# Optimization experiments

Measured on AMD Instinct MI355X. Metric: run time of the kernel, lower is better.

The kernel has to match this reference:

```python
import jax, jax.numpy as jnp
import numpy as np

F_IN = 22 * 1000   # flattened EEG trial
D_DENSE = 100      # Dense(100) -> becomes T=100 timesteps of dim 1
H = 128            # LSTM units
N_CLASS = 4


def setup_inputs() -> dict:
    key = jax.random.key(0)
    ks = jax.random.split(key, 8)
    B = 4096
    s1 = 1.0 / np.sqrt(F_IN)
    sr = 1.0 / np.sqrt(H)
    x = jax.random.normal(ks[0], (B, 22, 1000), dtype=jnp.float32)
    W1 = jax.random.uniform(ks[1], (F_IN, D_DENSE), jnp.float32, -s1, s1)
    b1 = jnp.zeros((D_DENSE,), jnp.float32)
    # Keras LSTM kernels: input kernel [1, 4H], recurrent kernel [H, 4H], bias [4H]
    Wk = jax.random.uniform(ks[2], (1, 4 * H), jnp.float32, -1.0, 1.0)
    Wr = jax.random.normal(ks[3], (H, 4 * H), dtype=jnp.float32) * sr
    # Keras unit_forget_bias: f-gate bias initialized to 1
    bl = jnp.concatenate([jnp.zeros(H), jnp.ones(H), jnp.zeros(2 * H)]).astype(jnp.float32)
    W2 = jax.random.uniform(ks[4], (H, N_CLASS), jnp.float32, -sr, sr)
    b2 = jnp.zeros((N_CLASS,), jnp.float32)
    return {"x": x, "W1": W1, "b1": b1, "Wk": Wk, "Wr": Wr, "bl": bl, "W2": W2, "b2": b2}


def _lstm_last(seq, Wk, Wr, bl):
    # seq: [B, T, 1]; returns final hidden state [B, H]
    B = seq.shape[0]
    # precompute input contribution for all steps: [T, B, 4H]
    zx = jnp.einsum('btf,fg->tbg', seq, Wk) + bl

    def step(carry, zxt):
        h, c = carry
        z = zxt + h @ Wr                      # [B, 4H]
        i, f, g, o = jnp.split(z, 4, axis=-1)  # keras gate order: i, f, c, o
        i = jax.nn.sigmoid(i)
        f = jax.nn.sigmoid(f)
        g = jnp.tanh(g)
        o = jax.nn.sigmoid(o)
        c = f * c + i * g
        h = o * jnp.tanh(c)
        return (h, c), None

    init = (jnp.zeros((B, H), seq.dtype), jnp.zeros((B, H), seq.dtype))
    (h, _), _ = jax.lax.scan(step, init, zx)
    return h


def reference(x, W1, b1, Wk, Wr, bl, W2, b2):
    B = x.shape[0]
    flat = x.reshape(B, -1)                 # Flatten
    d = flat @ W1 + b1                      # Dense(100), linear activation
    seq = d.reshape(B, D_DENSE, 1)          # Reshape((100, 1))
    h = _lstm_last(seq, Wk, Wr, bl)         # LSTM(128) -> last hidden state
    logits = h @ W2 + b2                    # Dense(4)
    return jax.nn.softmax(logits, axis=-1)
```

## Files before the change

### kernel.cpp

```cpp
#include <hip/hip_runtime.h>
#include <stdint.h>

#define F_IN   22000
#define B_SZ   4096
#define T_STEPS 100
#define NSPLIT 16
#define NCHUNK 22
#define KSPAN  (NCHUNK * 64)
#define ACC_STRIDE 104
#define PART_BYTES ((size_t)NSPLIT * B_SZ * ACC_STRIDE * 4)
#define BIMG_BYTES 28672
#define BIMG_HALF  14336
#define W1IMG_BYTES ((size_t)NSPLIT * NCHUNK * BIMG_BYTES)
#define WRIMG_BYTES (128 * 1024)
#define LOG2E  1.44269504f
#define LOG2E2 2.88539008f

typedef float f32x4 __attribute__((ext_vector_type(4)));
typedef short s16x8 __attribute__((ext_vector_type(8)));

__device__ inline unsigned short f2bf(float f){
  unsigned u = __builtin_bit_cast(unsigned, f);
  u += 0x7FFFu + ((u >> 16) & 1u);
  return (unsigned short)(u >> 16);
}
__device__ inline float bf2f(unsigned short h){
  return __builtin_bit_cast(float, ((unsigned)h) << 16);
}
__device__ inline float exp2f_(float x){
  float r; asm("v_exp_f32 %0, %1" : "=v"(r) : "v"(x)); return r;
}

__global__ __launch_bounds__(256) void k_prep(const float* __restrict__ W1,
                                              const float* __restrict__ Wr,
                                              char* __restrict__ img,
                                              char* __restrict__ wrimg){
  __shared__ float tile[64][129];
  int b = blockIdx.x, tid = threadIdx.x;
  if (b < 352){
    int ch = b % NCHUNK, s = b / NCHUNK;
    int k0 = s * KSPAN + ch * 64;
    char* base = img + ((size_t)(s * NCHUNK + ch)) * BIMG_BYTES;
    for (int idx = tid; idx < 64 * 128; idx += 256){
      int k = idx >> 7, c = idx & 127;
      float v = 0.f;
      if (c < 100 && (k0 + k) < F_IN) v = W1[(size_t)(k0 + k) * 100 + c];
      tile[k][c] = v;
    }
    __syncthreads();
    #pragma unroll
    for (int q = 0; q < 4; ++q){
      int task = q * 256 + tid;
      if (task < 896){
        int p  = task * 16;
        int c  = p >> 7;
        int k8 = ((p >> 4) & 7) ^ (c & 7);
        unsigned hw[4], lw[4];
        #pragma unroll
        for (int jj = 0; jj < 4; ++jj){
          float v0 = tile[k8 * 8 + jj * 2][c];
          float v1 = tile[k8 * 8 + jj * 2 + 1][c];
          unsigned short h0 = f2bf(v0), l0 = f2bf(v0 - bf2f(h0));
          unsigned short h1 = f2bf(v1), l1 = f2bf(v1 - bf2f(h1));
          hw[jj] = (unsigned)h0 | ((unsigned)h1 << 16);
          lw[jj] = (unsigned)l0 | ((unsigned)l1 << 16);
        }
        *(uint4*)(base + p)             = make_uint4(hw[0], hw[1], hw[2], hw[3]);
        *(uint4*)(base + BIMG_HALF + p) = make_uint4(lw[0], lw[1], lw[2], lw[3]);
      }
    }
  } else {
    int gid = (b - 352) * 256 + tid;
    int lane = gid & 63, slot = gid >> 6;
    int kk = slot & 3, G = (slot >> 2) & 3, w = slot >> 4;
    int oct = lane >> 4, lr = lane & 15;
    int col = G * 128 + w * 16 + lr;
    float sg = (G == 2) ? LOG2E2 : LOG2E;
    unsigned pk[4];
    #pragma unroll
    for (int jj = 0; jj < 4; ++jj){
      float v0 = Wr[(size_t)(kk * 32 + oct * 8 + jj * 2)     * 512 + col] * sg;
      float v1 = Wr[(size_t)(kk * 32 + oct * 8 + jj * 2 + 1) * 512 + col] * sg;
      pk[jj] = (unsigned)f2bf(v0) | ((unsigned)f2bf(v1) << 16);
    }
    *(uint4*)(wrimg + (size_t)gid * 16) = make_uint4(pk[0], pk[1], pk[2], pk[3]);
  }
}

__global__ __launch_bounds__(256, 4) void k_dense(const float* __restrict__ x,
                                                  const char* __restrict__ img,
                                                  float* __restrict__ part){
  __shared__ char Bb[BIMG_BYTES];
  int tid = threadIdx.x;
  int lane = tid & 63, w = tid >> 6;
  int r = lane & 15, oct = lane >> 4;
  int brow = blockIdx.x * 64;
  int s = blockIdx.y;
  int arow = brow + w * 16 + r;
  const float* xrow = x + (size_t)arow * F_IN;
  const char* isrc = img + (size_t)s * NCHUNK * BIMG_BYTES;
  int kbase = s * KSPAN;

  f32x4 acc[7];
  #pragma unroll
  for (int i = 0; i < 7; ++i) acc[i] = (f32x4)0.f;

  for (int ch = 0; ch < NCHUNK; ++ch){
    int k0 = kbase + ch * 64;
    int ka0 = k0 + oct * 8;
    int ka1 = k0 + 32 + oct * 8;
    float4 a0 = make_float4(0.f,0.f,0.f,0.f), a1 = a0, a2 = a0, a3 = a0;
    if (ka0 < F_IN){ a0 = *(const float4*)(xrow + ka0);
                     a1 = *(const float4*)(xrow + ka0 + 4); }
    if (ka1 < F_IN){ a2 = *(const float4*)(xrow + ka1);
                     a3 = *(const float4*)(xrow + ka1 + 4); }
    {
      const char* src = isrc + (size_t)ch * BIMG_BYTES;
      #pragma unroll
      for (int i = 0; i < 7; ++i){
        int seg = i * 4 + w;
        __builtin_amdgcn_global_load_lds(
          (const __attribute__((address_space(1))) void*)(src + seg * 1024 + lane * 16),
          (__attribute__((address_space(3))) void*)(Bb + seg * 1024), 16, 0, 0);
      }
    }
    __syncthreads();
    float va[16] = {a0.x,a0.y,a0.z,a0.w, a1.x,a1.y,a1.z,a1.w,
                    a2.x,a2.y,a2.z,a2.w, a3.x,a3.y,a3.z,a3.w};
    s16x8 ah0, al0, ah1, al1;
    #pragma unroll
    for (int j = 0; j < 8; ++j){
      unsigned short h = f2bf(va[j]);
      ah0[j] = (short)h; al0[j] = (short)f2bf(va[j] - bf2f(h));
    }
    #pragma unroll
    for (int j = 0; j < 8; ++j){
      unsigned short h = f2bf(va[8 + j]);
      ah1[j] = (short)h; al1[j] = (short)f2bf(va[8 + j] - bf2f(h));
    }
    #pragma unroll
    for (int ct = 0; ct < 7; ++ct){
      int c = ct * 16 + r;
      int byte0 = ((c * 128 + oct * 16) ^ ((c & 7) << 4));
      int byte1 = ((c * 128 + 64 + oct * 16) ^ ((c & 7) << 4));
      s16x8 bh0 = *(s16x8*)(Bb + byte0);
      s16x8 bl0 = *(s16x8*)(Bb + BIMG_HALF + byte0);
      s16x8 bh1 = *(s16x8*)(Bb + byte1);
      s16x8 bl1 = *(s16x8*)(Bb + BIMG_HALF + byte1);
      acc[ct] = __builtin_amdgcn_mfma_f32_16x16x32_bf16(ah0, bh0, acc[ct], 0, 0, 0);
      acc[ct] = __builtin_amdgcn_mfma_f32_16x16x32_bf16(ah0, bl0, acc[ct], 0, 0, 0);
      acc[ct] = __builtin_amdgcn_mfma_f32_16x16x32_bf16(al0, bh0, acc[ct], 0, 0, 0);
      acc[ct] = __builtin_amdgcn_mfma_f32_16x16x32_bf16(ah1, bh1, acc[ct], 0, 0, 0);
      acc[ct] = __builtin_amdgcn_mfma_f32_16x16x32_bf16(ah1, bl1, acc[ct], 0, 0, 0);
      acc[ct] = __builtin_amdgcn_mfma_f32_16x16x32_bf16(al1, bh1, acc[ct], 0, 0, 0);
    }
    __syncthreads();
  }

  float* pbase = part + (size_t)s * B_SZ * ACC_STRIDE;
  #pragma unroll
  for (int ct = 0; ct < 7; ++ct){
    int col = ct * 16 + r;
    if (col < 100){
      #pragma unroll
      for (int reg = 0; reg < 4; ++reg){
        int orow = brow + w * 16 + oct * 4 + reg;
        pbase[(size_t)orow * ACC_STRIDE + col] = acc[ct][reg];
      }
    }
  }
}

__global__ __launch_bounds__(512, 2) void k_lstm(const float* __restrict__ part,
                                                 const float* __restrict__ b1,
                                                 const float* __restrict__ Wk,
                                                 const char* __restrict__ wrimg,
                                                 const float* __restrict__ bl,
                                                 const float* __restrict__ W2,
                                                 const float* __restrict__ b2,
                                                 float* __restrict__ out){
  __shared__ unsigned short hbuf[2][16 * 128];
  __shared__ float dld[16][ACC_STRIDE];
  __shared__ float hf[16][132];
  int tid = threadIdx.x;
  int lane = tid & 63, w = tid >> 6;
  int oct = lane >> 4, lr = lane & 15;
  int brow = blockIdx.x * 16;

  for (int i = tid; i < 2048; i += 512) hbuf[0][i] = 0;
  for (int i = tid; i < 16 * T_STEPS; i += 512){
    int r = i / T_STEPS, t = i % T_STEPS;
    float v = b1[t];
    #pragma unroll
    for (int s = 0; s < NSPLIT; ++s)
      v += part[((size_t)(s * B_SZ + brow + r)) * ACC_STRIDE + t];
    dld[r][t] = v;
  }

  float wkv[4], blv[4];
  s16x8 bfrag[4][4];
  #pragma unroll
  for (int G = 0; G < 4; ++G){
    int col = G * 128 + w * 16 + lr;
    float sg = (G == 2) ? LOG2E2 : LOG2E;
    wkv[G] = Wk[col] * sg;
    blv[G] = bl[col] * sg;
    #pragma unroll
    for (int kk = 0; kk < 4; ++kk){
      bfrag[G][kk] = *(const s16x8*)(wrimg +
          ((size_t)(((w * 4 + G) * 4 + kk) * 64 + lane)) * 16);
    }
  }
  float cst[4];
  #pragma unroll
  for (int reg = 0; reg < 4; ++reg) cst[reg] = 0.f;
  int sxl = (2 * (((lr >> 2) + (lr & 3)) & 3) + ((lr >> 2) & 1)) << 4;
  __syncthreads();

  for (int t = 0; t < T_STEPS; ++t){
    int cur = t & 1;
    f32x4 accA[4], accB[4];
    float dv[4];
    #pragma unroll
    for (int reg = 0; reg < 4; ++reg) dv[reg] = dld[oct * 4 + reg][t];
    #pragma unroll
    for (int G = 0; G < 4; ++G){
      #pragma unroll
      for (int reg = 0; reg < 4; ++reg){
        accA[G][reg] = dv[reg] * wkv[G] + blv[G];
        accB[G][reg] = 0.f;
      }
    }
    #pragma unroll
    for (int kk = 0; kk < 4; ++kk){
      int abyte = (lr * 256 + kk * 64 + oct * 16) ^ sxl;
      s16x8 a = *(s16x8*)((char*)hbuf[cur] + abyte);
      if (kk < 2){
        #pragma unroll
        for (int G = 0; G < 4; ++G)
          accA[G] = __builtin_amdgcn_mfma_f32_16x16x32_bf16(a, bfrag[G][kk], accA[G], 0, 0, 0);
      } else {
        #pragma unroll
        for (int G = 0; G < 4; ++G)
          accB[G] = __builtin_amdgcn_mfma_f32_16x16x32_bf16(a, bfrag[G][kk], accB[G], 0, 0, 0);
      }
    }
    #pragma unroll
    for (int reg = 0; reg < 4; ++reg){
      float z0 = accA[0][reg] + accB[0][reg];
      float z1 = accA[1][reg] + accB[1][reg];
      float z2 = accA[2][reg] + accB[2][reg];
      float z3 = accA[3][reg] + accB[3][reg];
      float iv = __builtin_amdgcn_rcpf(1.f + exp2f_(-z0));
      float fv = __builtin_amdgcn_rcpf(1.f + exp2f_(-z1));
      float gv = 1.f - 2.f * __builtin_amdgcn_rcpf(exp2f_(z2) + 1.f);
      float ov = __builtin_amdgcn_rcpf(1.f + exp2f_(-z3));
      float cv = fv * cst[reg] + iv * gv;
      cst[reg] = cv;
      float tc = 1.f - 2.f * __builtin_amdgcn_rcpf(exp2f_(cv * LOG2E2) + 1.f);
      float hv = ov * tc;
      int row = oct * 4 + reg;
      int col = w * 16 + lr;
      int sw = (2 * ((oct + reg) & 3) + (oct & 1)) << 4;
      int byte = (row * 256 + col * 2) ^ sw;
      *(unsigned short*)((char*)hbuf[cur ^ 1] + byte) = f2bf(hv);
      if (t == T_STEPS - 1) hf[row][col] = hv;
    }
    __syncthreads();
  }

  if (tid < 64){
    int row = tid >> 2, cl = tid & 3;
    float a = b2[cl];
    #pragma unroll 8
    for (int j = 0; j < 128; ++j) a += hf[row][j] * W2[j * 4 + cl];
    float m = fmaxf(a, __shfl_xor(a, 1));
    m = fmaxf(m, __shfl_xor(m, 2));
    float e = __expf(a - m);
    float se = e + __shfl_xor(e, 1);
    se += __shfl_xor(se, 2);
    out[(size_t)(brow + row) * 4 + cl] = e * __builtin_amdgcn_rcpf(se);
  }
}

extern "C" void kernel_launch(void* const* d_in, const int* in_sizes, int n_in,
                              void* d_out, int out_size, void* d_ws, size_t ws_size,
                              hipStream_t stream){
  const float* x  = (const float*)d_in[0];
  const float* W1 = (const float*)d_in[1];
  const float* b1 = (const float*)d_in[2];
  const float* Wk = (const float*)d_in[3];
  const float* Wr = (const float*)d_in[4];
  const float* bl = (const float*)d_in[5];
  const float* W2 = (const float*)d_in[6];
  const float* b2 = (const float*)d_in[7];
  float* out = (float*)d_out;

  char* ws = (char*)d_ws;
  float* part  = (float*)ws;
  char*  img   = ws + PART_BYTES;
  char*  wrimg = ws + PART_BYTES + W1IMG_BYTES;

  k_prep<<<384, 256, 0, stream>>>(W1, Wr, img, wrimg);
  k_dense<<<dim3(B_SZ / 64, NSPLIT), 256, 0, stream>>>(x, img, part);
  k_lstm<<<B_SZ / 16, 512, 0, stream>>>(part, b1, Wk, wrimg, bl, W2, b2, out);
}
```

Baseline: 232.2 us.

## Retune dense K-split and occupancy, prefetch LSTM inputs, drop final-h buffer

The dense GEMM K-split goes from 16x22 chunks to 20x18 chunks, giving more blocks and shorter K spans, and k_dense's occupancy hint rises from 4 to 5 blocks per CU. In the LSTM kernel, the per-step dense input is prefetched one step ahead, and the swizzle offsets are hoisted out of the loop. Negation is folded into the v_exp_f32 source modifier, and the fp32 final-hidden buffer is removed, so the classifier head reads the bf16 hidden state from hbuf. Costs are more partial-sum traffic in the LSTM prologue, possible register pressure from the higher occupancy target, and bf16 rather than fp32 final hidden values feeding the head.

Result: slower. 243.8 us (+5.0%).

```diff
diff --git a/kernel.cpp b/kernel.cpp
--- a/kernel.cpp
+++ b/kernel.cpp
@@ -4,8 +4,8 @@
 #define F_IN   22000
 #define B_SZ   4096
 #define T_STEPS 100
-#define NSPLIT 16
-#define NCHUNK 22
+#define NSPLIT 20
+#define NCHUNK 18
 #define KSPAN  (NCHUNK * 64)
 #define ACC_STRIDE 104
 #define PART_BYTES ((size_t)NSPLIT * B_SZ * ACC_STRIDE * 4)
@@ -30,6 +30,9 @@
 __device__ inline float exp2f_(float x){
   float r; asm("v_exp_f32 %0, %1" : "=v"(r) : "v"(x)); return r;
 }
+__device__ inline float exp2n_(float x){
+  float r; asm("v_exp_f32 %0, -%1" : "=v"(r) : "v"(x)); return r;
+}
 
 __global__ __launch_bounds__(256) void k_prep(const float* __restrict__ W1,
                                               const float* __restrict__ Wr,
@@ -37,7 +40,7 @@
                                               char* __restrict__ wrimg){
   __shared__ float tile[64][129];
   int b = blockIdx.x, tid = threadIdx.x;
-  if (b < 352){
+  if (b < NSPLIT * NCHUNK){
     int ch = b % NCHUNK, s = b / NCHUNK;
     int k0 = s * KSPAN + ch * 64;
     char* base = img + ((size_t)(s * NCHUNK + ch)) * BIMG_BYTES;
@@ -70,7 +73,7 @@
       }
     }
   } else {
-    int gid = (b - 352) * 256 + tid;
+    int gid = (b - NSPLIT * NCHUNK) * 256 + tid;
     int lane = gid & 63, slot = gid >> 6;
     int kk = slot & 3, G = (slot >> 2) & 3, w = slot >> 4;
     int oct = lane >> 4, lr = lane & 15;
@@ -87,7 +90,7 @@
   }
 }
 
-__global__ __launch_bounds__(256, 4) void k_dense(const float* __restrict__ x,
+__global__ __launch_bounds__(256, 5) void k_dense(const float* __restrict__ x,
                                                   const char* __restrict__ img,
                                                   float* __restrict__ part){
   __shared__ char Bb[BIMG_BYTES];
@@ -181,7 +184,6 @@
                                                  float* __restrict__ out){
   __shared__ unsigned short hbuf[2][16 * 128];
   __shared__ float dld[16][ACC_STRIDE];
-  __shared__ float hf[16][132];
   int tid = threadIdx.x;
   int lane = tid & 63, w = tid >> 6;
   int oct = lane >> 4, lr = lane & 15;
@@ -215,14 +217,19 @@
   #pragma unroll
   for (int reg = 0; reg < 4; ++reg) cst[reg] = 0.f;
   int sxl = (2 * (((lr >> 2) + (lr & 3)) & 3) + ((lr >> 2) & 1)) << 4;
+  int sxw[4];
+  #pragma unroll
+  for (int reg = 0; reg < 4; ++reg)
+    sxw[reg] = (2 * ((oct + reg) & 3) + (oct & 1)) << 4;
   __syncthreads();
+
+  float dv[4];
+  #pragma unroll
+  for (int reg = 0; reg < 4; ++reg) dv[reg] = dld[oct * 4 + reg][0];
 
   for (int t = 0; t < T_STEPS; ++t){
     int cur = t & 1;
     f32x4 accA[4], accB[4];
-    float dv[4];
-    #pragma unroll
-    for (int reg = 0; reg < 4; ++reg) dv[reg] = dld[oct * 4 + reg][t];
     #pragma unroll
     for (int G = 0; G < 4; ++G){
       #pragma unroll
@@ -231,6 +238,11 @@
         accB[G][reg] = 0.f;
       }
     }
+    float dvn[4];
+    int tn = (t + 1 < T_STEPS) ? t + 1 : t;
+    #pragma unroll
+    for (int reg = 0; reg < 4; ++reg) dvn[reg] = dld[oct * 4 + reg][tn];
+
     #pragma unroll
     for (int kk = 0; kk < 4; ++kk){
       int abyte = (lr * 256 + kk * 64 + oct * 16) ^ sxl;
@@ -251,29 +263,33 @@
       float z1 = accA[1][reg] + accB[1][reg];
       float z2 = accA[2][reg] + accB[2][reg];
       float z3 = accA[3][reg] + accB[3][reg];
-      float iv = __builtin_amdgcn_rcpf(1.f + exp2f_(-z0));
-      float fv = __builtin_amdgcn_rcpf(1.f + exp2f_(-z1));
+      float iv = __builtin_amdgcn_rcpf(1.f + exp2n_(z0));
+      float fv = __builtin_amdgcn_rcpf(1.f + exp2n_(z1));
       float gv = 1.f - 2.f * __builtin_amdgcn_rcpf(exp2f_(z2) + 1.f);
-      float ov = __builtin_amdgcn_rcpf(1.f + exp2f_(-z3));
+      float ov = __builtin_amdgcn_rcpf(1.f + exp2n_(z3));
       float cv = fv * cst[reg] + iv * gv;
       cst[reg] = cv;
       float tc = 1.f - 2.f * __builtin_amdgcn_rcpf(exp2f_(cv * LOG2E2) + 1.f);
       float hv = ov * tc;
       int row = oct * 4 + reg;
       int col = w * 16 + lr;
-      int sw = (2 * ((oct + reg) & 3) + (oct & 1)) << 4;
-      int byte = (row * 256 + col * 2) ^ sw;
+      int byte = (row * 256 + col * 2) ^ sxw[reg];
       *(unsigned short*)((char*)hbuf[cur ^ 1] + byte) = f2bf(hv);
-      if (t == T_STEPS - 1) hf[row][col] = hv;
-    }
+    }
+    #pragma unroll
+    for (int reg = 0; reg < 4; ++reg) dv[reg] = dvn[reg];
     __syncthreads();
   }
 
   if (tid < 64){
     int row = tid >> 2, cl = tid & 3;
+    int sxr = (2 * (((row >> 2) + (row & 3)) & 3) + ((row >> 2) & 1)) << 4;
     float a = b2[cl];
     #pragma unroll 8
-    for (int j = 0; j < 128; ++j) a += hf[row][j] * W2[j * 4 + cl];
+    for (int j = 0; j < 128; ++j){
+      int byte = (row * 256 + j * 2) ^ sxr;
+      a += bf2f(*(unsigned short*)((char*)hbuf[0] + byte)) * W2[j * 4 + cl];
+    }
     float m = fmaxf(a, __shfl_xor(a, 1));
     m = fmaxf(m, __shfl_xor(m, 2));
     float e = __expf(a - m);
@@ -301,7 +317,7 @@
   char*  img   = ws + PART_BYTES;
   char*  wrimg = ws + PART_BYTES + W1IMG_BYTES;
 
-  k_prep<<<384, 256, 0, stream>>>(W1, Wr, img, wrimg);
+  k_prep<<<NSPLIT * NCHUNK + 32, 256, 0, stream>>>(W1, Wr, img, wrimg);
   k_dense<<<dim3(B_SZ / 64, NSPLIT), 256, 0, stream>>>(x, img, part);
   k_lstm<<<B_SZ / 16, 512, 0, stream>>>(part, b1, Wk, wrimg, bl, W2, b2, out);
 }
```
